# Kernel tuning notes

Hardware: AMD Instinct MI355X
Metric: run time of the kernel (lower is better)

The kernel has to match this reference:

```python
import jax, jax.numpy as jnp
import numpy as np

B, D, C = 1024, 128, 100000
EPS = 1e-12  # torch F.normalize eps


def setup_inputs() -> dict:
    key = jax.random.key(0)
    k1, k2, k3 = jax.random.split(key, 3)
    # scale so ||x||^2 ~ 1, keeping exp(-dist) in a representable range
    xs = jax.random.normal(k1, (B, D), dtype=jnp.float32) / np.sqrt(D)
    ys = jax.random.randint(k2, (B,), 0, C, dtype=jnp.int64)
    # xavier_uniform init of Embedding(C, D): U(-a, a), a = sqrt(6/(C+D))
    a = np.sqrt(6.0 / (C + D))
    proxies = jax.random.uniform(k3, (C, D), dtype=jnp.float32, minval=-a, maxval=a)
    return {"xs": xs, "ys": ys, "proxies": proxies}


def reference(xs, ys, proxies):
    # L2-normalize every proxy (original normalizes pos proxy over dim=0 of a 1-D
    # vector and neg proxies over dim=1 -- both are per-proxy L2 normalization).
    norm = jnp.linalg.norm(proxies, axis=1, keepdims=True)
    P = proxies / jnp.maximum(norm, EPS)                      # [C, D], unit rows
    x_sq = jnp.sum(xs * xs, axis=1, keepdims=True)            # [B, 1]
    d = x_sq + 1.0 - 2.0 * (xs @ P.T)                         # [B, C]
    e = jnp.exp(-d)                                           # [B, C]
    pos = jnp.take_along_axis(e, ys[:, None], axis=1)[:, 0]   # exp(-d[b, y_b])
    neg_sum = jnp.sum(e, axis=1) - pos                        # denominator excludes the positive
    return jnp.mean(-jnp.log(pos / neg_sum))
```

## Files before the change

kernel.cpp:

```cpp
#include <hip/hip_runtime.h>
#include <hip/hip_fp16.h>

#define B_N 1024
#define D_K 128
#define C_N 100000
#define CCHUNK 80
#define NCC 1250
#define BSPLIT 2
#define NBLK_MAIN (NCC * BSPLIT)
#define NREP 8
#define EPSN 1e-12f
#define XSCL 2.8853900817779268f

typedef _Float16 half8 __attribute__((ext_vector_type(8)));
typedef float floatx4 __attribute__((ext_vector_type(4)));

union U16 { uint4 u; half8 h; };

#if __has_builtin(__builtin_amdgcn_exp2f)
__device__ __forceinline__ float exp2_hw(float x) { return __builtin_amdgcn_exp2f(x); }
#else
__device__ __forceinline__ float exp2_hw(float x) {
    float r; asm("v_exp_f32 %0, %1" : "=v"(r) : "v"(x)); return r;
}
#endif

__device__ __forceinline__ unsigned int pack2h(float a, float b) {
    union { _Float16 h[2]; unsigned int u; } p;
    p.h[0] = (_Float16)a; p.h[1] = (_Float16)b;
    return p.u;
}

__global__ __launch_bounds__(256) void prep_kernel(
    const float* __restrict__ xs, const int* __restrict__ ys,
    const float* __restrict__ proxies,
    unsigned int* __restrict__ xfrag, float* __restrict__ w,
    float* __restrict__ posd, float* __restrict__ negsumR)
{
    int tid  = threadIdx.x;
    int gid  = blockIdx.x * 256 + tid;
    if (gid < B_N * NREP) negsumR[gid] = 0.0f;

    int wave = tid >> 6, lane = tid & 63;
    int b = blockIdx.x * 4 + wave;

    const float2 xv = ((const float2*)(xs + (size_t)b * D_K))[lane];
    float ss = xv.x * xv.x + xv.y * xv.y;
    #pragma unroll
    for (int m = 1; m < 64; m <<= 1) ss += __shfl_xor(ss, m, 64);
    float xsq = ss;

    {
        int f  = lane >> 4;
        int m4 = (lane >> 2) & 3;
        int j  = lane & 3;
        int idx = ((((b >> 4) * 4 + f) * 64) + ((b & 15) | (m4 << 4))) * 4 + j;
        xfrag[idx] = pack2h(XSCL * xv.x, XSCL * xv.y);
    }

    int y = ys[b];
    const float2 pv = ((const float2*)(proxies + (size_t)y * D_K))[lane];
    float dt = xv.x * pv.x + xv.y * pv.y;
    float pp = pv.x * pv.x + pv.y * pv.y;
    #pragma unroll
    for (int m = 1; m < 64; m <<= 1) {
        dt += __shfl_xor(dt, m, 64);
        pp += __shfl_xor(pp, m, 64);
    }
    if (lane == 0) {
        w[b] = __expf(-xsq - 1.0f);
        float nrm = fmaxf(sqrtf(pp), EPSN);
        posd[b] = xsq + 1.0f - 2.0f * (dt / nrm);
    }
}

__device__ __forceinline__ void stage_row(
    uint4* __restrict__ lp,
    float4 v0, float4 v1, float4 v2, float4 v3, int r, int L)
{
    float ss = v0.x*v0.x + v0.y*v0.y + v0.z*v0.z + v0.w*v0.w
             + v1.x*v1.x + v1.y*v1.y + v1.z*v1.z + v1.w*v1.w
             + v2.x*v2.x + v2.y*v2.y + v2.z*v2.z + v2.w*v2.w
             + v3.x*v3.x + v3.y*v3.y + v3.z*v3.z + v3.w*v3.w;
    ss += __shfl_xor(ss, 1, 64);
    ss += __shfl_xor(ss, 2, 64);
    ss += __shfl_xor(ss, 4, 64);
    float sc = 1.0f / fmaxf(sqrtf(ss), EPSN);

    union { _Float16 h[8]; uint4 u; } pa, pb;
    pa.h[0]=(_Float16)(v0.x*sc); pa.h[1]=(_Float16)(v0.y*sc);
    pa.h[2]=(_Float16)(v0.z*sc); pa.h[3]=(_Float16)(v0.w*sc);
    pa.h[4]=(_Float16)(v1.x*sc); pa.h[5]=(_Float16)(v1.y*sc);
    pa.h[6]=(_Float16)(v1.z*sc); pa.h[7]=(_Float16)(v1.w*sc);
    pb.h[0]=(_Float16)(v2.x*sc); pb.h[1]=(_Float16)(v2.y*sc);
    pb.h[2]=(_Float16)(v2.z*sc); pb.h[3]=(_Float16)(v2.w*sc);
    pb.h[4]=(_Float16)(v3.x*sc); pb.h[5]=(_Float16)(v3.y*sc);
    pb.h[6]=(_Float16)(v3.z*sc); pb.h[7]=(_Float16)(v3.w*sc);

    int cb = r >> 4, rc = r & 15;
    int f  = L >> 1;
    int mA = (L * 2) & 3;
    int mB = (L * 2 + 1) & 3;
    lp[(cb * 4 + f) * 64 + (rc | (mA << 4))] = pa.u;
    lp[(cb * 4 + f) * 64 + (rc | (mB << 4))] = pb.u;
}

__global__ __launch_bounds__(256, 4) void main_kernel(
    const float* __restrict__ proxies,
    const uint4* __restrict__ xfrag,
    float* __restrict__ negsumR)
{
    __shared__ uint4 ldsP[CCHUNK * 16];

    int tid = threadIdx.x;
    int bx  = blockIdx.x;
    int cc  = bx >> 1;
    int bs  = bx & 1;
    int c0  = cc * CCHUNK;

    {
        int L  = tid & 7;
        int rb = tid >> 3;
        const float* base = proxies + (size_t)c0 * D_K + L * 16;
        const float4* s0 = (const float4*)(base + (size_t)rb * D_K);
        const float4* s1 = (const float4*)(base + (size_t)(rb + 32) * D_K);
        float4 A0 = s0[0], A1 = s0[1], A2 = s0[2], A3 = s0[3];
        float4 B0 = s1[0], B1 = s1[1], B2 = s1[2], B3 = s1[3];
        float4 C0, C1, C2, C3;
        if (rb < 16) {
            const float4* s2 = (const float4*)(base + (size_t)(rb + 64) * D_K);
            C0 = s2[0]; C1 = s2[1]; C2 = s2[2]; C3 = s2[3];
        }
        stage_row(ldsP, A0, A1, A2, A3, rb,      L);
        stage_row(ldsP, B0, B1, B2, B3, rb + 32, L);
        if (rb < 16)
            stage_row(ldsP, C0, C1, C2, C3, rb + 64, L);
    }
    __syncthreads();

    int wave  = tid >> 6, lane = tid & 63;
    int b0    = bs * 512 + wave * 128;
    int t0    = b0 >> 4;
    float* nsr = negsumR + (size_t)(bx & (NREP - 1)) * B_N;

    #pragma unroll 1
    for (int bg = 0; bg < 4; ++bg) {
        uint4 xf[2][4];
        #pragma unroll
        for (int bt = 0; bt < 2; ++bt)
            #pragma unroll
            for (int f = 0; f < 4; ++f)
                xf[bt][f] = xfrag[((t0 + bg * 2 + bt) * 4 + f) * 64 + lane];

        float sv[2] = {0.f, 0.f};

        #pragma unroll 1
        for (int cb = 0; cb < CCHUNK / 16; ++cb) {
            uint4 a[4];
            #pragma unroll
            for (int f = 0; f < 4; ++f)
                a[f] = ldsP[(cb * 4 + f) * 64 + lane];

            #pragma unroll
            for (int bt = 0; bt < 2; ++bt) {
                floatx4 acc = {0.f, 0.f, 0.f, 0.f};
                #pragma unroll
                for (int f = 0; f < 4; ++f) {
                    U16 ua, ub;
                    ua.u = a[f];
                    ub.u = xf[bt][f];
                    acc = __builtin_amdgcn_mfma_f32_16x16x32_f16(ua.h, ub.h, acc, 0, 0, 0);
                }
                float e0 = exp2_hw(acc[0]), e1 = exp2_hw(acc[1]);
                float e2 = exp2_hw(acc[2]), e3 = exp2_hw(acc[3]);
                sv[bt] += (e0 + e1) + (e2 + e3);
            }
        }

        #pragma unroll
        for (int bt = 0; bt < 2; ++bt) {
            float v = sv[bt];
            v += __shfl_xor(v, 16, 64);
            v += __shfl_xor(v, 32, 64);
            if (lane < 16)
                atomicAdd(&nsr[b0 + bg * 32 + bt * 16 + lane], v);
        }
    }
}

__global__ __launch_bounds__(1024) void final_kernel(
    const float* __restrict__ negsumR, const float* __restrict__ w,
    const float* __restrict__ posd, float* __restrict__ out)
{
    __shared__ float red[1024];
    int t = threadIdx.x;
    float ns = 0.0f;
    #pragma unroll
    for (int r = 0; r < NREP; ++r) ns += negsumR[r * B_N + t];
    float pd = posd[t];
    red[t] = logf(ns * w[t] - __expf(-pd)) + pd;
    __syncthreads();
    #pragma unroll
    for (int s = 512; s > 0; s >>= 1) {
        if (t < s) red[t] += red[t + s];
        __syncthreads();
    }
    if (t == 0) out[0] = red[0] * (1.0f / 1024.0f);
}

extern "C" void kernel_launch(void* const* d_in, const int* in_sizes, int n_in,
                              void* d_out, int out_size, void* d_ws, size_t ws_size,
                              hipStream_t stream)
{
    const float* xs      = (const float*)d_in[0];
    const int*   ys      = (const int*)d_in[1];
    const float* proxies = (const float*)d_in[2];

    char* ws = (char*)d_ws;
    unsigned int* xfrag = (unsigned int*)ws;
    float* w       = (float*)(ws + 262144);
    float* posd    = (float*)(ws + 262144 + 4096);
    float* negsumR = (float*)(ws + 262144 + 8192);

    prep_kernel<<<256, 256, 0, stream>>>(xs, ys, proxies, xfrag, w, posd, negsumR);
    main_kernel<<<NBLK_MAIN, 256, 0, stream>>>(proxies, (const uint4*)ws, negsumR);
    final_kernel<<<1, 1024, 0, stream>>>(negsumR, w, posd, (float*)d_out);
}
```

Baseline: 118.1 us.

## Double-buffer x fragments and LDS tiles, interleave MFMAs, swizzle LDS layout

```diff
diff --git a/kernel.cpp b/kernel.cpp
--- a/kernel.cpp
+++ b/kernel.cpp
@@ -101,9 +101,54 @@
     int f  = L >> 1;
     int mA = (L * 2) & 3;
     int mB = (L * 2 + 1) & 3;
-    lp[(cb * 4 + f) * 64 + (rc | (mA << 4))] = pa.u;
-    lp[(cb * 4 + f) * 64 + (rc | (mB << 4))] = pb.u;
-}
+    lp[(cb * 4 + f) * 64 + (((rc | (mA << 4))) ^ f)] = pa.u;
+    lp[(cb * 4 + f) * 64 + (((rc | (mB << 4))) ^ f)] = pb.u;
+}
+
+#define LOAD_XF(DST, BGI) do {                                              \
+    _Pragma("unroll")                                                       \
+    for (int bt = 0; bt < 2; ++bt)                                          \
+        _Pragma("unroll")                                                   \
+        for (int f = 0; f < 4; ++f)                                         \
+            DST[bt][f] = xfrag[((t0 + (BGI) * 2 + bt) * 4 + f) * 64 + lane];\
+} while (0)
+
+#define MFMA_EXP(AC, XF, SV0, SV1) do {                                     \
+    floatx4 acc0 = {0.f,0.f,0.f,0.f}, acc1 = {0.f,0.f,0.f,0.f};             \
+    _Pragma("unroll")                                                       \
+    for (int f = 0; f < 4; ++f) {                                           \
+        U16 ua, u0, u1;                                                     \
+        ua.u = AC[f]; u0.u = XF[0][f]; u1.u = XF[1][f];                     \
+        acc0 = __builtin_amdgcn_mfma_f32_16x16x32_f16(ua.h, u0.h, acc0, 0, 0, 0); \
+        acc1 = __builtin_amdgcn_mfma_f32_16x16x32_f16(ua.h, u1.h, acc1, 0, 0, 0); \
+    }                                                                       \
+    SV0 += (exp2_hw(acc0[0]) + exp2_hw(acc0[1]))                            \
+         + (exp2_hw(acc0[2]) + exp2_hw(acc0[3]));                           \
+    SV1 += (exp2_hw(acc1[0]) + exp2_hw(acc1[1]))                            \
+         + (exp2_hw(acc1[2]) + exp2_hw(acc1[3]));                           \
+} while (0)
+
+#define COMPUTE_BG(XF, BGI) do {                                            \
+    float sv0 = 0.f, sv1 = 0.f;                                             \
+    uint4 ac[4], an[4];                                                     \
+    _Pragma("unroll")                                                       \
+    for (int f = 0; f < 4; ++f) ac[f] = ldsP[offF[f]];                      \
+    _Pragma("unroll 1")                                                     \
+    for (int cb = 0; cb < 4; ++cb) {                                        \
+        _Pragma("unroll")                                                   \
+        for (int f = 0; f < 4; ++f) an[f] = ldsP[(cb + 1) * 256 + offF[f]]; \
+        MFMA_EXP(ac, XF, sv0, sv1);                                         \
+        _Pragma("unroll")                                                   \
+        for (int f = 0; f < 4; ++f) ac[f] = an[f];                          \
+    }                                                                       \
+    MFMA_EXP(ac, XF, sv0, sv1);                                             \
+    sv0 += __shfl_xor(sv0, 16, 64); sv0 += __shfl_xor(sv0, 32, 64);         \
+    sv1 += __shfl_xor(sv1, 16, 64); sv1 += __shfl_xor(sv1, 32, 64);         \
+    if (lane < 16) {                                                        \
+        atomicAdd(&nsr[b0 + (BGI) * 32 + lane],      sv0);                  \
+        atomicAdd(&nsr[b0 + (BGI) * 32 + 16 + lane], sv1);                  \
+    }                                                                       \
+} while (0)
 
 __global__ __launch_bounds__(256, 4) void main_kernel(
     const float* __restrict__ proxies,
@@ -143,48 +188,19 @@
     int t0    = b0 >> 4;
     float* nsr = negsumR + (size_t)(bx & (NREP - 1)) * B_N;
 
+    int offF[4];
+    #pragma unroll
+    for (int f = 0; f < 4; ++f) offF[f] = f * 64 + (lane ^ f);
+
+    uint4 xfA[2][4], xfB[2][4];
+    LOAD_XF(xfA, 0);
+
     #pragma unroll 1
-    for (int bg = 0; bg < 4; ++bg) {
-        uint4 xf[2][4];
-        #pragma unroll
-        for (int bt = 0; bt < 2; ++bt)
-            #pragma unroll
-            for (int f = 0; f < 4; ++f)
-                xf[bt][f] = xfrag[((t0 + bg * 2 + bt) * 4 + f) * 64 + lane];
-
-        float sv[2] = {0.f, 0.f};
-
-        #pragma unroll 1
-        for (int cb = 0; cb < CCHUNK / 16; ++cb) {
-            uint4 a[4];
-            #pragma unroll
-            for (int f = 0; f < 4; ++f)
-                a[f] = ldsP[(cb * 4 + f) * 64 + lane];
-
-            #pragma unroll
-            for (int bt = 0; bt < 2; ++bt) {
-                floatx4 acc = {0.f, 0.f, 0.f, 0.f};
-                #pragma unroll
-                for (int f = 0; f < 4; ++f) {
-                    U16 ua, ub;
-                    ua.u = a[f];
-                    ub.u = xf[bt][f];
-                    acc = __builtin_amdgcn_mfma_f32_16x16x32_f16(ua.h, ub.h, acc, 0, 0, 0);
-                }
-                float e0 = exp2_hw(acc[0]), e1 = exp2_hw(acc[1]);
-                float e2 = exp2_hw(acc[2]), e3 = exp2_hw(acc[3]);
-                sv[bt] += (e0 + e1) + (e2 + e3);
-            }
-        }
-
-        #pragma unroll
-        for (int bt = 0; bt < 2; ++bt) {
-            float v = sv[bt];
-            v += __shfl_xor(v, 16, 64);
-            v += __shfl_xor(v, 32, 64);
-            if (lane < 16)
-                atomicAdd(&nsr[b0 + bg * 32 + bt * 16 + lane], v);
-        }
+    for (int bgp = 0; bgp < 2; ++bgp) {
+        LOAD_XF(xfB, bgp * 2 + 1);
+        COMPUTE_BG(xfA, bgp * 2);
+        if (bgp == 0) LOAD_XF(xfA, 2);
+        COMPUTE_BG(xfB, bgp * 2 + 1);
     }
 }
 
```

Measured after the change: 127.3 us. +7.8%, slower.
